# Optimization experiments

Hardware: AMD Instinct MI355X
Metric: run time of the kernel (lower is better)

Reference implementation:

```python
import jax, jax.numpy as jnp
import numpy as np

DIM = 1024
INNER = DIM // 2
DSTATE = 8
KSZ = 3
DTRANK = max(INNER // 8, 4)
B, L = 4, 4096


def setup_inputs() -> dict:
    key = jax.random.key(0)
    ks = jax.random.split(key, 8)
    s = 0.02
    x = jax.random.normal(ks[0], (B, L, DIM), dtype=jnp.float32)
    W_in = jax.random.normal(ks[1], (DIM, DIM), dtype=jnp.float32) * s
    Kx = jax.random.normal(ks[2], (INNER, 1, KSZ), dtype=jnp.float32) * 0.1
    Kz = jax.random.normal(ks[3], (INNER, 1, KSZ), dtype=jnp.float32) * 0.1
    W_xproj = jax.random.normal(ks[4], (DTRANK + 2 * DSTATE, INNER), dtype=jnp.float32) * s
    W_dt = jax.random.normal(ks[5], (INNER, DTRANK), dtype=jnp.float32) * s
    # dt bias: inverse_softplus of exp(linspace(log dt_min, log dt_max))
    dt_init = jnp.exp(jnp.linspace(jnp.log(0.02), jnp.log(0.2), INNER))
    b_dt = jnp.log(jnp.expm1(dt_init)).astype(jnp.float32)
    A_log = jnp.log(jnp.tile(jnp.arange(1, DSTATE + 1, dtype=jnp.float32), (INNER, 1)))
    D = jnp.ones((INNER,), dtype=jnp.float32)
    W_out = jax.random.normal(ks[6], (DIM, DIM), dtype=jnp.float32) * s
    return {"x": x, "W_in": W_in, "Kx": Kx, "Kz": Kz, "W_xproj": W_xproj,
            "W_dt": W_dt, "b_dt": b_dt, "A_log": A_log, "D": D, "W_out": W_out}


def _dwconv_silu(u, kern):
    # u: [B,L,C], kern: [C,1,K] depthwise (groups=C), 'same' padding
    c = u.shape[-1]
    v = jnp.transpose(u, (0, 2, 1))  # [B,C,L]
    v = jax.lax.conv_general_dilated(v, kern, (1,), [(KSZ // 2, KSZ // 2)],
                                     dimension_numbers=("NCH", "OIH", "NCH"),
                                     feature_group_count=c)
    return jax.nn.silu(jnp.transpose(v, (0, 2, 1)))


def _forward(x, W_in, Kx, Kz, W_xproj, W_dt, b_dt, A_log, D, W_out):
    h = jnp.einsum("bld,ed->ble", x, W_in)  # Linear(dim,dim), no bias
    xb, zb = jnp.split(h, 2, axis=-1)       # [B,L,INNER] each
    xb = _dwconv_silu(xb, Kx)
    zb = _dwconv_silu(zb, Kz)
    proj = jnp.einsum("blc,oc->blo", xb, W_xproj)
    dt_raw = proj[..., :DTRANK]
    b_raw = proj[..., DTRANK:DTRANK + DSTATE]
    c_raw = proj[..., DTRANK + DSTATE:]
    delta = jnp.clip(jax.nn.softplus(jnp.einsum("blr,cr->blc", dt_raw, W_dt) + b_dt), 1e-4, 1.0)  # [B,L,C]
    b_term = jnp.tanh(b_raw)  # [B,L,N]
    c_term = jnp.tanh(c_raw)  # [B,L,N]
    a = jax.nn.softplus(A_log) + 1e-4  # [C,N]
    decay = jnp.clip(jnp.exp(-delta[..., None] * a), 1e-4, 1.0)        # [B,L,C,N]
    drive = (1.0 - decay) * (b_term[:, :, None, :] * xb[..., None])    # [B,L,C,N]

    def step(state, inp):
        dec_t, drv_t, c_t, x_t = inp  # [B,C,N], [B,C,N], [B,N], [B,C]
        state = dec_t * state + drv_t
        y = jnp.sum(state * c_t[:, None, :], axis=-1) + D * x_t  # [B,C]
        return state, y

    tm = lambda t: jnp.moveaxis(t, 1, 0)  # time-major
    state0 = jnp.zeros((x.shape[0], INNER, DSTATE), dtype=jnp.float32)
    _, ys = jax.lax.scan(step, state0, (tm(decay), tm(drive), tm(c_term), tm(xb)))
    y = jnp.moveaxis(ys, 0, 1)  # [B,L,INNER]
    return jnp.einsum("bld,ed->ble", jnp.concatenate([y, zb], axis=-1), W_out)


def reference(x, W_in, Kx, Kz, W_xproj, W_dt, b_dt, A_log, D, W_out):
    return _forward(x, W_in, Kx, Kz, W_xproj, W_dt, b_dt, A_log, D, W_out)
```

## Files before the change

kernel.cpp:

```cpp
#include <hip/hip_runtime.h>


using bf16x8 = __attribute__((ext_vector_type(8))) short;
using f32x4  = __attribute__((ext_vector_type(4))) float;

__device__ __forceinline__ unsigned short f2bf(float f) {
  unsigned int u = __float_as_uint(f);
  u = u + 0x7fffu + ((u >> 16) & 1u);
  return (unsigned short)(u >> 16);
}

__device__ __forceinline__ float fsoftplus(float x) {
  return (x > 15.f) ? x : __logf(1.f + __expf(x));
}

__device__ __forceinline__ float ftanh(float x) {
  float v = fminf(fmaxf(x, -15.f), 15.f);
  float e = __expf(2.f * v);
  return (e - 1.f) / (e + 1.f);
}

__global__ __launch_bounds__(256) void cvt_bf16_kernel(
    const float* __restrict__ in, unsigned short* __restrict__ out, int n4) {
  int i = blockIdx.x * 256 + threadIdx.x;
  if (i < n4) {
    float4 v = ((const float4*)in)[i];
    ushort4 o;
    o.x = f2bf(v.x); o.y = f2bf(v.y); o.z = f2bf(v.z); o.w = f2bf(v.w);
    ((ushort4*)out)[i] = o;
  }
}

__global__ __launch_bounds__(256) void cvt_wxp_kernel(
    const float* __restrict__ Wx, unsigned short* __restrict__ out) {
  int i = blockIdx.x * 256 + threadIdx.x;
  int row = i >> 9;
  out[i] = (row < 80) ? f2bf(Wx[i]) : (unsigned short)0;
}

__global__ __launch_bounds__(256) void gemm_bt_bf16(
    const unsigned short* __restrict__ A,
    const unsigned short* __restrict__ B,
    float* __restrict__ C, int M, int N, int K) {
  __shared__ short As[128 * 32];
  __shared__ short Bs[128 * 32];
  const int m0 = blockIdx.x * 128;
  const int n0 = blockIdx.y * 128;
  const int lane = threadIdx.x & 63;
  const int wv = threadIdx.x >> 6;
  const int wm = (wv >> 1) * 64;
  const int wn = (wv & 1) * 64;
  f32x4 acc[4][4] = {};
  const int row_a = wv * 32 + (lane >> 2);
  const int koff = (lane & 3) * 8;
  const unsigned short* gA = A + (size_t)(m0 + row_a) * K + koff;
  const unsigned short* gB = B + (size_t)(n0 + row_a) * K + koff;
  short* lA = &As[(wv * 32) * 32];
  short* lB = &Bs[(wv * 32) * 32];
  const int r = lane & 15;
  const int q = lane >> 4;
  for (int k0 = 0; k0 < K; k0 += 32) {
    __syncthreads();
    __builtin_amdgcn_global_load_lds((const __attribute__((address_space(1))) void*)(const void*)gA,
                                     (__attribute__((address_space(3))) void*)(void*)lA, 16, 0, 0);
    __builtin_amdgcn_global_load_lds((const __attribute__((address_space(1))) void*)(const void*)(gA + 16 * K),
                                     (__attribute__((address_space(3))) void*)(void*)(lA + 16 * 32), 16, 0, 0);
    __builtin_amdgcn_global_load_lds((const __attribute__((address_space(1))) void*)(const void*)gB,
                                     (__attribute__((address_space(3))) void*)(void*)lB, 16, 0, 0);
    __builtin_amdgcn_global_load_lds((const __attribute__((address_space(1))) void*)(const void*)(gB + 16 * K),
                                     (__attribute__((address_space(3))) void*)(void*)(lB + 16 * 32), 16, 0, 0);
    gA += 32; gB += 32;
    __syncthreads();
    bf16x8 av[4], bv[4];
#pragma unroll
    for (int i = 0; i < 4; ++i)
      av[i] = *(const bf16x8*)&As[(wm + i * 16 + r) * 32 + q * 8];
#pragma unroll
    for (int j = 0; j < 4; ++j)
      bv[j] = *(const bf16x8*)&Bs[(wn + j * 16 + r) * 32 + q * 8];
#pragma unroll
    for (int i = 0; i < 4; ++i)
#pragma unroll
      for (int j = 0; j < 4; ++j)
        acc[i][j] = __builtin_amdgcn_mfma_f32_16x16x32_bf16(av[i], bv[j], acc[i][j], 0, 0, 0);
  }
#pragma unroll
  for (int i = 0; i < 4; ++i)
#pragma unroll
    for (int j = 0; j < 4; ++j)
#pragma unroll
      for (int t = 0; t < 4; ++t)
        C[(size_t)(m0 + wm + i * 16 + q * 4 + t) * N + (n0 + wn + j * 16 + r)] = acc[i][j][t];
}

__global__ __launch_bounds__(256) void conv_silu_kernel(
    const float* __restrict__ h, const float* __restrict__ Kx, const float* __restrict__ Kz,
    float* __restrict__ xb, unsigned short* __restrict__ xbbf,
    unsigned short* __restrict__ cat) {
  int tid = blockIdx.x * 256 + threadIdx.x;
  int ch = tid & 1023;
  int bl = tid >> 10;
  int l = bl & 4095;
  float k0, k1, k2;
  int c;
  if (ch < 512) { c = ch;       k0 = Kx[c * 3]; k1 = Kx[c * 3 + 1]; k2 = Kx[c * 3 + 2]; }
  else          { c = ch - 512; k0 = Kz[c * 3]; k1 = Kz[c * 3 + 1]; k2 = Kz[c * 3 + 2]; }
  size_t idx = (size_t)bl * 1024 + ch;
  float um = (l > 0)    ? h[idx - 1024] : 0.f;
  float u0 = h[idx];
  float up = (l < 4095) ? h[idx + 1024] : 0.f;
  float v = um * k0 + u0 * k1 + up * k2;
  float o = v / (1.f + __expf(-v));
  if (ch < 512) { xb[(size_t)bl * 512 + c] = o; xbbf[(size_t)bl * 512 + c] = f2bf(o); }
  else          cat[idx] = f2bf(o);
}

__global__ __launch_bounds__(256) void prep_dtbc_kernel(
    const float* __restrict__ proj, unsigned short* __restrict__ dtr,
    float* __restrict__ bterm, float* __restrict__ cterm) {
  int i = blockIdx.x * 256 + threadIdx.x;
  int row = i >> 7, col = i & 127;
  float v = proj[i];
  if (col < 64)      dtr[row * 64 + col] = f2bf(v);
  else if (col < 72) bterm[row * 8 + (col - 64)] = ftanh(v);
  else if (col < 80) cterm[row * 8 + (col - 72)] = ftanh(v);
}

__global__ __launch_bounds__(256) void scan_p1(
    const float* __restrict__ draw, const float* __restrict__ bterm,
    const float* __restrict__ xb, const float* __restrict__ A_log,
    const float* __restrict__ bdt,
    float* __restrict__ Aprod, float* __restrict__ Bpart) {
  int tid = threadIdx.x;
  int gid = blockIdx.x;
  int chunk = gid & 127, half = (gid >> 7) & 1, b = gid >> 8;
  int c = half * 256 + tid;
  float4 a0 = *(const float4*)&A_log[c * 8];
  float4 a1 = *(const float4*)&A_log[c * 8 + 4];
  float na[8] = {a0.x, a0.y, a0.z, a0.w, a1.x, a1.y, a1.z, a1.w};
#pragma unroll
  for (int s = 0; s < 8; ++s) na[s] = -(fsoftplus(na[s]) + 1e-4f);
  float bb = bdt[c];
  int l0 = chunk * 32;
  size_t base  = ((size_t)b * 4096 + l0) * 512 + c;
  size_t bbase = ((size_t)b * 4096 + l0) * 8;
  float S[8] = {}, Ap[8] = {1.f, 1.f, 1.f, 1.f, 1.f, 1.f, 1.f, 1.f};
  for (int i = 0; i < 32; ++i) {
    float dr = draw[base] + bb;
    float xv = xb[base];
    float delta = fminf(fmaxf(fsoftplus(dr), 1e-4f), 1.f);
    float4 bt0 = *(const float4*)&bterm[bbase];
    float4 bt1 = *(const float4*)&bterm[bbase + 4];
    float bt[8] = {bt0.x, bt0.y, bt0.z, bt0.w, bt1.x, bt1.y, bt1.z, bt1.w};
#pragma unroll
    for (int s = 0; s < 8; ++s) {
      float dec = fminf(fmaxf(__expf(delta * na[s]), 1e-4f), 1.f);
      float btx = bt[s] * xv;
      S[s] = dec * S[s] + (btx - dec * btx);
      Ap[s] *= dec;
    }
    base += 512; bbase += 8;
  }
  size_t o = (size_t)chunk * 16384 + ((size_t)(b * 512 + c)) * 8;
  *(float4*)&Aprod[o]     = make_float4(Ap[0], Ap[1], Ap[2], Ap[3]);
  *(float4*)&Aprod[o + 4] = make_float4(Ap[4], Ap[5], Ap[6], Ap[7]);
  *(float4*)&Bpart[o]     = make_float4(S[0], S[1], S[2], S[3]);
  *(float4*)&Bpart[o + 4] = make_float4(S[4], S[5], S[6], S[7]);
}

__global__ __launch_bounds__(256) void scan_p2(
    const float* __restrict__ Aprod, const float* __restrict__ Bpart,
    float* __restrict__ initst) {
  int t = blockIdx.x * 256 + threadIdx.x;
  float st = 0.f;
  for (int ch = 0; ch < 128; ++ch) {
    size_t o = (size_t)ch * 16384 + t;
    initst[o] = st;
    st = Aprod[o] * st + Bpart[o];
  }
}

__global__ __launch_bounds__(256) void scan_p3(
    const float* __restrict__ draw, const float* __restrict__ bterm,
    const float* __restrict__ cterm, const float* __restrict__ xb,
    const float* __restrict__ A_log, const float* __restrict__ bdt,
    const float* __restrict__ Dp,
    const float* __restrict__ initst, unsigned short* __restrict__ cat) {
  int tid = threadIdx.x;
  int gid = blockIdx.x;
  int chunk = gid & 127, half = (gid >> 7) & 1, b = gid >> 8;
  int c = half * 256 + tid;
  float4 a0 = *(const float4*)&A_log[c * 8];
  float4 a1 = *(const float4*)&A_log[c * 8 + 4];
  float na[8] = {a0.x, a0.y, a0.z, a0.w, a1.x, a1.y, a1.z, a1.w};
#pragma unroll
  for (int s = 0; s < 8; ++s) na[s] = -(fsoftplus(na[s]) + 1e-4f);
  float bb = bdt[c];
  float Dv = Dp[c];
  size_t o = (size_t)chunk * 16384 + ((size_t)(b * 512 + c)) * 8;
  float4 s0 = *(const float4*)&initst[o];
  float4 s1 = *(const float4*)&initst[o + 4];
  float S[8] = {s0.x, s0.y, s0.z, s0.w, s1.x, s1.y, s1.z, s1.w};
  int l0 = chunk * 32;
  size_t base  = ((size_t)b * 4096 + l0) * 512 + c;
  size_t bbase = ((size_t)b * 4096 + l0) * 8;
  size_t cbase = ((size_t)b * 4096 + l0) * 1024 + c;
  for (int i = 0; i < 32; ++i) {
    float dr = draw[base] + bb;
    float xv = xb[base];
    float delta = fminf(fmaxf(fsoftplus(dr), 1e-4f), 1.f);
    float4 bt0 = *(const float4*)&bterm[bbase];
    float4 bt1 = *(const float4*)&bterm[bbase + 4];
    float4 ct0 = *(const float4*)&cterm[bbase];
    float4 ct1 = *(const float4*)&cterm[bbase + 4];
    float bt[8] = {bt0.x, bt0.y, bt0.z, bt0.w, bt1.x, bt1.y, bt1.z, bt1.w};
    float ct[8] = {ct0.x, ct0.y, ct0.z, ct0.w, ct1.x, ct1.y, ct1.z, ct1.w};
    float acc = Dv * xv;
#pragma unroll
    for (int s = 0; s < 8; ++s) {
      float dec = fminf(fmaxf(__expf(delta * na[s]), 1e-4f), 1.f);
      float btx = bt[s] * xv;
      S[s] = dec * S[s] + (btx - dec * btx);
      acc += S[s] * ct[s];
    }
    cat[cbase] = f2bf(acc);
    base += 512; bbase += 8; cbase += 1024;
  }
}

extern "C" void kernel_launch(void* const* d_in, const int* in_sizes, int n_in,
                              void* d_out, int out_size, void* d_ws, size_t ws_size,
                              hipStream_t stream) {
  (void)in_sizes; (void)n_in; (void)out_size; (void)ws_size;
  const float* x       = (const float*)d_in[0];
  const float* W_in    = (const float*)d_in[1];
  const float* Kx      = (const float*)d_in[2];
  const float* Kz      = (const float*)d_in[3];
  const float* W_xproj = (const float*)d_in[4];
  const float* W_dt    = (const float*)d_in[5];
  const float* b_dt    = (const float*)d_in[6];
  const float* A_log   = (const float*)d_in[7];
  const float* Dp      = (const float*)d_in[8];
  const float* W_out   = (const float*)d_in[9];
  float* out = (float*)d_out;

  char* w = (char*)d_ws;
  unsigned short* xbf  = (unsigned short*)(w);
  float* xb    = (float*)(w + 33554432);
  float* draw  = (float*)(w + 67108864);
  float* bterm = (float*)(w + 100663296);
  float* cterm = (float*)(w + 101187584);
  float* Aprod = (float*)(w + 101711872);
  float* Bpart = (float*)(w + 110100480);
  float* initst = (float*)(w + 118489088);
  unsigned short* winbf  = (unsigned short*)(w + 126877696);
  unsigned short* woutbf = (unsigned short*)(w + 128974848);
  unsigned short* dtr    = (unsigned short*)(w + 131072000);
  unsigned short* wxp_bf = (unsigned short*)(w + 133169152);
  unsigned short* wd_bf  = (unsigned short*)(w + 133300224);
  unsigned short* xbbf = (unsigned short*)Aprod;
  float* proj = draw;
  float* h = out;

  cvt_bf16_kernel<<<16384, 256, 0, stream>>>(x, xbf, 4194304);
  cvt_bf16_kernel<<<1024, 256, 0, stream>>>(W_in, winbf, 262144);
  cvt_bf16_kernel<<<1024, 256, 0, stream>>>(W_out, woutbf, 262144);
  cvt_bf16_kernel<<<32, 256, 0, stream>>>(W_dt, wd_bf, 8192);
  cvt_wxp_kernel<<<256, 256, 0, stream>>>(W_xproj, wxp_bf);

  gemm_bt_bf16<<<dim3(128, 8), 256, 0, stream>>>(xbf, winbf, h, 16384, 1024, 1024);

  conv_silu_kernel<<<65536, 256, 0, stream>>>(h, Kx, Kz, xb, xbbf, xbf );

  gemm_bt_bf16<<<dim3(128, 1), 256, 0, stream>>>(xbbf, wxp_bf, proj, 16384, 128, 512);
  prep_dtbc_kernel<<<8192, 256, 0, stream>>>(proj, dtr, bterm, cterm);
  gemm_bt_bf16<<<dim3(128, 4), 256, 0, stream>>>(dtr, wd_bf, draw, 16384, 512, 64);

  scan_p1<<<1024, 256, 0, stream>>>(draw, bterm, xb, A_log, b_dt, Aprod, Bpart);
  scan_p2<<<64, 256, 0, stream>>>(Aprod, Bpart, initst);
  scan_p3<<<1024, 256, 0, stream>>>(draw, bterm, cterm, xb, A_log, b_dt, Dp, initst, xbf );

  gemm_bt_bf16<<<dim3(128, 8), 256, 0, stream>>>(xbf, woutbf, out, 16384, 1024, 1024);
}
```

Baseline: 371.2 us.

## Store GEMM intermediates as bf16 and rework LDS tile layout

The input-projection GEMM and the dt GEMM now write bf16 rather than fp32. The conv kernel reads bf16 h and no longer writes an fp32 xb copy, and the scan kernels read bf16 draw and xb. Together these cut the bytes moved through HBM in the memory-bound elementwise and scan stages. The GEMM's shared-memory staging is also reorganised into k-slice-major blocks, which changes both the global load pattern and the LDS read bank pattern. In exchange, the intermediate activations lose precision.

```diff
diff --git a/kernel.cpp b/kernel.cpp
--- a/kernel.cpp
+++ b/kernel.cpp
@@ -8,6 +8,9 @@
   unsigned int u = __float_as_uint(f);
   u = u + 0x7fffu + ((u >> 16) & 1u);
   return (unsigned short)(u >> 16);
+}
+__device__ __forceinline__ float bf2f(unsigned short u) {
+  return __uint_as_float(((unsigned int)u) << 16);
 }
 
 __device__ __forceinline__ float fsoftplus(float x) {
@@ -38,12 +41,13 @@
   out[i] = (row < 80) ? f2bf(Wx[i]) : (unsigned short)0;
 }
 
-__global__ __launch_bounds__(256) void gemm_bt_bf16(
+template <bool BF16OUT>
+__global__ __launch_bounds__(256) void gemm_bt(
     const unsigned short* __restrict__ A,
     const unsigned short* __restrict__ B,
-    float* __restrict__ C, int M, int N, int K) {
-  __shared__ short As[128 * 32];
-  __shared__ short Bs[128 * 32];
+    void* __restrict__ Cp, int M, int N, int K) {
+  __shared__ short As[4096];
+  __shared__ short Bs[4096];
   const int m0 = blockIdx.x * 128;
   const int n0 = blockIdx.y * 128;
   const int lane = threadIdx.x & 63;
@@ -51,33 +55,35 @@
   const int wm = (wv >> 1) * 64;
   const int wn = (wv & 1) * 64;
   f32x4 acc[4][4] = {};
-  const int row_a = wv * 32 + (lane >> 2);
-  const int koff = (lane & 3) * 8;
-  const unsigned short* gA = A + (size_t)(m0 + row_a) * K + koff;
-  const unsigned short* gB = B + (size_t)(n0 + row_a) * K + koff;
-  short* lA = &As[(wv * 32) * 32];
-  short* lB = &Bs[(wv * 32) * 32];
+  const unsigned short* gA0 = A + (size_t)(m0 + lane) * K + wv * 8;
+  const unsigned short* gA1 = A + (size_t)(m0 + 64 + lane) * K + wv * 8;
+  const unsigned short* gB0 = B + (size_t)(n0 + lane) * K + wv * 8;
+  const unsigned short* gB1 = B + (size_t)(n0 + 64 + lane) * K + wv * 8;
+  short* lA0 = &As[wv * 1024];
+  short* lA1 = &As[wv * 1024 + 512];
+  short* lB0 = &Bs[wv * 1024];
+  short* lB1 = &Bs[wv * 1024 + 512];
   const int r = lane & 15;
   const int q = lane >> 4;
   for (int k0 = 0; k0 < K; k0 += 32) {
     __syncthreads();
-    __builtin_amdgcn_global_load_lds((const __attribute__((address_space(1))) void*)(const void*)gA,
-                                     (__attribute__((address_space(3))) void*)(void*)lA, 16, 0, 0);
-    __builtin_amdgcn_global_load_lds((const __attribute__((address_space(1))) void*)(const void*)(gA + 16 * K),
-                                     (__attribute__((address_space(3))) void*)(void*)(lA + 16 * 32), 16, 0, 0);
-    __builtin_amdgcn_global_load_lds((const __attribute__((address_space(1))) void*)(const void*)gB,
-                                     (__attribute__((address_space(3))) void*)(void*)lB, 16, 0, 0);
-    __builtin_amdgcn_global_load_lds((const __attribute__((address_space(1))) void*)(const void*)(gB + 16 * K),
-                                     (__attribute__((address_space(3))) void*)(void*)(lB + 16 * 32), 16, 0, 0);
-    gA += 32; gB += 32;
+    __builtin_amdgcn_global_load_lds((const __attribute__((address_space(1))) void*)(const void*)gA0,
+                                     (__attribute__((address_space(3))) void*)(void*)lA0, 16, 0, 0);
+    __builtin_amdgcn_global_load_lds((const __attribute__((address_space(1))) void*)(const void*)gA1,
+                                     (__attribute__((address_space(3))) void*)(void*)lA1, 16, 0, 0);
+    __builtin_amdgcn_global_load_lds((const __attribute__((address_space(1))) void*)(const void*)gB0,
+                                     (__attribute__((address_space(3))) void*)(void*)lB0, 16, 0, 0);
+    __builtin_amdgcn_global_load_lds((const __attribute__((address_space(1))) void*)(const void*)gB1,
+                                     (__attribute__((address_space(3))) void*)(void*)lB1, 16, 0, 0);
+    gA0 += 32; gA1 += 32; gB0 += 32; gB1 += 32;
     __syncthreads();
     bf16x8 av[4], bv[4];
 #pragma unroll
     for (int i = 0; i < 4; ++i)
-      av[i] = *(const bf16x8*)&As[(wm + i * 16 + r) * 32 + q * 8];
+      av[i] = *(const bf16x8*)&As[q * 1024 + (wm + i * 16 + r) * 8];
 #pragma unroll
     for (int j = 0; j < 4; ++j)
-      bv[j] = *(const bf16x8*)&Bs[(wn + j * 16 + r) * 32 + q * 8];
+      bv[j] = *(const bf16x8*)&Bs[q * 1024 + (wn + j * 16 + r) * 8];
 #pragma unroll
     for (int i = 0; i < 4; ++i)
 #pragma unroll
@@ -89,14 +95,17 @@
 #pragma unroll
     for (int j = 0; j < 4; ++j)
 #pragma unroll
-      for (int t = 0; t < 4; ++t)
-        C[(size_t)(m0 + wm + i * 16 + q * 4 + t) * N + (n0 + wn + j * 16 + r)] = acc[i][j][t];
+      for (int t = 0; t < 4; ++t) {
+        size_t off = (size_t)(m0 + wm + i * 16 + q * 4 + t) * N + (n0 + wn + j * 16 + r);
+        if (BF16OUT) ((unsigned short*)Cp)[off] = f2bf(acc[i][j][t]);
+        else         ((float*)Cp)[off] = acc[i][j][t];
+      }
 }
 
 __global__ __launch_bounds__(256) void conv_silu_kernel(
-    const float* __restrict__ h, const float* __restrict__ Kx, const float* __restrict__ Kz,
-    float* __restrict__ xb, unsigned short* __restrict__ xbbf,
-    unsigned short* __restrict__ cat) {
+    const unsigned short* __restrict__ h, const float* __restrict__ Kx,
+    const float* __restrict__ Kz,
+    unsigned short* __restrict__ xbbf, unsigned short* __restrict__ cat) {
   int tid = blockIdx.x * 256 + threadIdx.x;
   int ch = tid & 1023;
   int bl = tid >> 10;
@@ -106,12 +115,12 @@
   if (ch < 512) { c = ch;       k0 = Kx[c * 3]; k1 = Kx[c * 3 + 1]; k2 = Kx[c * 3 + 2]; }
   else          { c = ch - 512; k0 = Kz[c * 3]; k1 = Kz[c * 3 + 1]; k2 = Kz[c * 3 + 2]; }
   size_t idx = (size_t)bl * 1024 + ch;
-  float um = (l > 0)    ? h[idx - 1024] : 0.f;
-  float u0 = h[idx];
-  float up = (l < 4095) ? h[idx + 1024] : 0.f;
+  float um = (l > 0)    ? bf2f(h[idx - 1024]) : 0.f;
+  float u0 = bf2f(h[idx]);
+  float up = (l < 4095) ? bf2f(h[idx + 1024]) : 0.f;
   float v = um * k0 + u0 * k1 + up * k2;
   float o = v / (1.f + __expf(-v));
-  if (ch < 512) { xb[(size_t)bl * 512 + c] = o; xbbf[(size_t)bl * 512 + c] = f2bf(o); }
+  if (ch < 512) xbbf[(size_t)bl * 512 + c] = f2bf(o);
   else          cat[idx] = f2bf(o);
 }
 
@@ -127,8 +136,8 @@
 }
 
 __global__ __launch_bounds__(256) void scan_p1(
-    const float* __restrict__ draw, const float* __restrict__ bterm,
-    const float* __restrict__ xb, const float* __restrict__ A_log,
+    const unsigned short* __restrict__ draw, const float* __restrict__ bterm,
+    const unsigned short* __restrict__ xb, const float* __restrict__ A_log,
     const float* __restrict__ bdt,
     float* __restrict__ Aprod, float* __restrict__ Bpart) {
   int tid = threadIdx.x;
@@ -146,8 +155,8 @@
   size_t bbase = ((size_t)b * 4096 + l0) * 8;
   float S[8] = {}, Ap[8] = {1.f, 1.f, 1.f, 1.f, 1.f, 1.f, 1.f, 1.f};
   for (int i = 0; i < 32; ++i) {
-    float dr = draw[base] + bb;
-    float xv = xb[base];
+    float dr = bf2f(draw[base]) + bb;
+    float xv = bf2f(xb[base]);
     float delta = fminf(fmaxf(fsoftplus(dr), 1e-4f), 1.f);
     float4 bt0 = *(const float4*)&bterm[bbase];
     float4 bt1 = *(const float4*)&bterm[bbase + 4];
@@ -181,8 +190,8 @@
 }
 
 __global__ __launch_bounds__(256) void scan_p3(
-    const float* __restrict__ draw, const float* __restrict__ bterm,
-    const float* __restrict__ cterm, const float* __restrict__ xb,
+    const unsigned short* __restrict__ draw, const float* __restrict__ bterm,
+    const float* __restrict__ cterm, const unsigned short* __restrict__ xb,
     const float* __restrict__ A_log, const float* __restrict__ bdt,
     const float* __restrict__ Dp,
     const float* __restrict__ initst, unsigned short* __restrict__ cat) {
@@ -206,8 +215,8 @@
   size_t bbase = ((size_t)b * 4096 + l0) * 8;
   size_t cbase = ((size_t)b * 4096 + l0) * 1024 + c;
   for (int i = 0; i < 32; ++i) {
-    float dr = draw[base] + bb;
-    float xv = xb[base];
+    float dr = bf2f(draw[base]) + bb;
+    float xv = bf2f(xb[base]);
     float delta = fminf(fmaxf(fsoftplus(dr), 1e-4f), 1.f);
     float4 bt0 = *(const float4*)&bterm[bbase];
     float4 bt1 = *(const float4*)&bterm[bbase + 4];
@@ -245,22 +254,21 @@
   float* out = (float*)d_out;
 
   char* w = (char*)d_ws;
-  unsigned short* xbf  = (unsigned short*)(w);
-  float* xb    = (float*)(w + 33554432);
-  float* draw  = (float*)(w + 67108864);
-  float* bterm = (float*)(w + 100663296);
-  float* cterm = (float*)(w + 101187584);
-  float* Aprod = (float*)(w + 101711872);
-  float* Bpart = (float*)(w + 110100480);
-  float* initst = (float*)(w + 118489088);
-  unsigned short* winbf  = (unsigned short*)(w + 126877696);
-  unsigned short* woutbf = (unsigned short*)(w + 128974848);
-  unsigned short* dtr    = (unsigned short*)(w + 131072000);
-  unsigned short* wxp_bf = (unsigned short*)(w + 133169152);
-  unsigned short* wd_bf  = (unsigned short*)(w + 133300224);
-  unsigned short* xbbf = (unsigned short*)Aprod;
-  float* proj = draw;
-  float* h = out;
+  unsigned short* xbf    = (unsigned short*)(w);
+  unsigned short* draw16 = (unsigned short*)(w + 33554432);
+  float* bterm  = (float*)(w + 50331648);
+  float* cterm  = (float*)(w + 50855936);
+  float* Aprod  = (float*)(w + 51380224);
+  float* Bpart  = (float*)(w + 59768832);
+  float* initst = (float*)(w + 68157440);
+  unsigned short* winbf  = (unsigned short*)(w + 76546048);
+  unsigned short* woutbf = (unsigned short*)(w + 78643200);
+  unsigned short* dtr    = (unsigned short*)(w + 80740352);
+  unsigned short* wxp_bf = (unsigned short*)(w + 82837504);
+  unsigned short* wd_bf  = (unsigned short*)(w + 82968576);
+  unsigned short* xbbf   = (unsigned short*)(w + 83034112);
+  float* proj            = (float*)(w + 99811328);
+  unsigned short* h = (unsigned short*)out;
 
   cvt_bf16_kernel<<<16384, 256, 0, stream>>>(x, xbf, 4194304);
   cvt_bf16_kernel<<<1024, 256, 0, stream>>>(W_in, winbf, 262144);
@@ -268,17 +276,17 @@
   cvt_bf16_kernel<<<32, 256, 0, stream>>>(W_dt, wd_bf, 8192);
   cvt_wxp_kernel<<<256, 256, 0, stream>>>(W_xproj, wxp_bf);
 
-  gemm_bt_bf16<<<dim3(128, 8), 256, 0, stream>>>(xbf, winbf, h, 16384, 1024, 1024);
-
-  conv_silu_kernel<<<65536, 256, 0, stream>>>(h, Kx, Kz, xb, xbbf, xbf );
-
-  gemm_bt_bf16<<<dim3(128, 1), 256, 0, stream>>>(xbbf, wxp_bf, proj, 16384, 128, 512);
+  gemm_bt<true><<<dim3(128, 8), 256, 0, stream>>>(xbf, winbf, h, 16384, 1024, 1024);
+
+  conv_silu_kernel<<<65536, 256, 0, stream>>>(h, Kx, Kz, xbbf, xbf );
+
+  gemm_bt<false><<<dim3(128, 1), 256, 0, stream>>>(xbbf, wxp_bf, proj, 16384, 128, 512);
   prep_dtbc_kernel<<<8192, 256, 0, stream>>>(proj, dtr, bterm, cterm);
-  gemm_bt_bf16<<<dim3(128, 4), 256, 0, stream>>>(dtr, wd_bf, draw, 16384, 512, 64);
-
-  scan_p1<<<1024, 256, 0, stream>>>(draw, bterm, xb, A_log, b_dt, Aprod, Bpart);
+  gemm_bt<true><<<dim3(128, 4), 256, 0, stream>>>(dtr, wd_bf, draw16, 16384, 512, 64);
+
+  scan_p1<<<1024, 256, 0, stream>>>(draw16, bterm, xbbf, A_log, b_dt, Aprod, Bpart);
   scan_p2<<<64, 256, 0, stream>>>(Aprod, Bpart, initst);
-  scan_p3<<<1024, 256, 0, stream>>>(draw, bterm, cterm, xb, A_log, b_dt, Dp, initst, xbf );
-
-  gemm_bt_bf16<<<dim3(128, 8), 256, 0, stream>>>(xbf, woutbf, out, 16384, 1024, 1024);
-}
+  scan_p3<<<1024, 256, 0, stream>>>(draw16, bterm, cterm, xbbf, A_log, b_dt, Dp, initst, xbf );
+
+  gemm_bt<false><<<dim3(128, 8), 256, 0, stream>>>(xbf, woutbf, out, 16384, 1024, 1024);
+}
```

New measurement: 431.8 us. 1.16x slower.
